# Optimization experiments

Hardware: AMD Instinct MI355X
Metric: run time of the kernel (lower is better)

Reference implementation:

```python
import math
import jax, jax.numpy as jnp
import numpy as np

L = 3
EPS = 1e-06


def _geometry(H, W, L):
    """Replicates the Python-side region layout of the torch ramac() exactly."""
    ovr = 0.4
    steps = np.array([2, 3, 4, 5, 6, 7], dtype=np.float64)
    w = min(W, H)
    b = (max(H, W) - w) / (steps - 1)
    idx = int(np.argmin(np.abs((w ** 2 - w * b) / w ** 2 - ovr)))
    Wd = idx if H < W else 0
    Hd = idx if H > W else 0
    regions = []  # list of (i, j, wl) static ints
    for l in range(1, L + 1):
        wl = math.floor(2 * w / (l + 1))
        if wl == 0:
            continue
        wl2 = math.floor(wl / 2 - 1)
        bW = 0 if l + Wd == 1 else (W - wl) / (l + Wd - 1)
        cenW = [int(math.floor(wl2 + k * bW) - wl2) for k in range(l - 1 + Wd + 1)]
        bH = 0 if l + Hd == 1 else (H - wl) / (l + Hd - 1)
        cenH = [int(math.floor(wl2 + k * bH) - wl2) for k in range(l - 1 + Hd + 1)]
        for i in cenH:
            for j in cenW:
                regions.append((i, j, wl))
    return regions


def _weighted_mac(R, tt_region, eps):
    # R: [B, C, h, w]; tt_region: [B, h, w] bool
    vt = R.max(axis=(2, 3))  # [B, C] regional max-pool
    area = tt_region.shape[-2] * tt_region.shape[-1]
    # NOTE: faithful to torch: sum over batch too, divided only by region area
    wgt = tt_region.sum().astype(jnp.float32) / area
    wgt = jnp.where(wgt <= 1.0 / 3.0, jnp.zeros_like(wgt), wgt)
    nrm = jnp.linalg.norm(vt, axis=1, keepdims=True)  # L2 over channels
    return vt / (nrm + eps) * wgt


def _ramac(x, L, eps):
    B, C, H, W = x.shape
    s = x.sum(axis=1)                 # [B, H, W]
    tt = (s - s.mean()) > 0           # [B, H, W] attention mask (bool)
    v = _weighted_mac(x, tt, eps)     # global region
    for (i, j, wl) in _geometry(H, W, L):
        R = x[:, :, i:i + wl, j:j + wl]
        v = v + _weighted_mac(R, tt[:, i:i + wl, j:j + wl], eps)
    return v.reshape(B, C, 1, 1)


def setup_inputs() -> dict:
    key = jax.random.key(0)
    x = jax.random.normal(key, (16, 1024, 64, 64), dtype=jnp.float32)
    return {"x": x}


def reference(x):
    return _ramac(x, L, EPS)
```

## Files before the change

### kernel.cpp

```cpp
#include <hip/hip_runtime.h>
#include <math.h>


#define NB 16
#define NC 1024
#define HW 4096
#define NF4 1024
#define G 16
#define NCHUNK (NC / G)

template <int ctrl, int rm, int bm>
__device__ __forceinline__ float maxdpp(float x) {
  int xi = __float_as_int(x);
  int yi = __builtin_amdgcn_update_dpp(xi, xi, ctrl, rm, bm, false);
  return fmaxf(x, __int_as_float(yi));
}
__device__ __forceinline__ float wave_max64(float x) {
  x = maxdpp<0x111, 0xf, 0xf>(x);
  x = maxdpp<0x112, 0xf, 0xf>(x);
  x = maxdpp<0x114, 0xf, 0xe>(x);
  x = maxdpp<0x118, 0xf, 0xc>(x);
  x = maxdpp<0x142, 0xa, 0xf>(x);
  x = maxdpp<0x143, 0x8, 0xf>(x);
  return x;
}

__global__ __launch_bounds__(256) void k1_main(
    const float4* __restrict__ x, float* __restrict__ vtp,
    float4* __restrict__ spart4, float* __restrict__ total,
    int* __restrict__ cnt) {
  const int t = threadIdx.x;
  const int chunk = blockIdx.x;
  const int b = blockIdx.y;
  if (chunk == 0 && b == 0) {
    if (t == 0) *total = 0.f;
    if (t < 14) cnt[t] = 0;
  }
  const int fb = t & 15;
  const int r0 = t >> 4;
  const int w = t >> 6;
  const float NEG = -INFINITY;
  const bool cAf = (fb <= 9), cAp = (fb == 10);
  const bool cBf = (fb >= 6), cBp = (fb == 5);
  const bool cCm = (fb < 8);
  const bool cDm = (fb >= 4) && (fb < 12);
  const bool cEm = (fb >= 8);
  const bool rAk2 = (r0 < 10);
  const bool rBk1 = (r0 >= 6);

  float4 sa0 = {0, 0, 0, 0}, sa1 = {0, 0, 0, 0}, sa2 = {0, 0, 0, 0},
         sa3 = {0, 0, 0, 0};
  const float4* img = x + (((size_t)(b * NC + chunk * G)) << 10);

  for (int ci = 0; ci < G; ++ci) {
    const float4* p = img + (((size_t)ci) << 10);
    float4 v0 = p[t], v1 = p[t + 256], v2 = p[t + 512], v3 = p[t + 768];
    sa0.x += v0.x; sa0.y += v0.y; sa0.z += v0.z; sa0.w += v0.w;
    sa1.x += v1.x; sa1.y += v1.y; sa1.z += v1.z; sa1.w += v1.w;
    sa2.x += v2.x; sa2.y += v2.y; sa2.z += v2.z; sa2.w += v2.w;
    sa3.x += v3.x; sa3.y += v3.y; sa3.z += v3.z; sa3.w += v3.w;

    float m0 = fmaxf(fmaxf(v0.x, v0.y), fmaxf(v0.z, v0.w));
    float m1 = fmaxf(fmaxf(v1.x, v1.y), fmaxf(v1.z, v1.w));
    float m2 = fmaxf(fmaxf(v2.x, v2.y), fmaxf(v2.z, v2.w));
    float m3 = fmaxf(fmaxf(v3.x, v3.y), fmaxf(v3.z, v3.w));
    float pA0 = fmaxf(v0.x, v0.y), pA1 = fmaxf(v1.x, v1.y);
    float pA2 = fmaxf(v2.x, v2.y), pA3 = fmaxf(v3.x, v3.y);
    float pB0 = fmaxf(v0.z, v0.w), pB1 = fmaxf(v1.z, v1.w);
    float pB2 = fmaxf(v2.z, v2.w), pB3 = fmaxf(v3.z, v3.w);

    float cA0 = cAf ? m0 : (cAp ? pA0 : NEG);
    float cA1 = cAf ? m1 : (cAp ? pA1 : NEG);
    float cA2 = cAf ? m2 : (cAp ? pA2 : NEG);
    float cA3 = cAf ? m3 : (cAp ? pA3 : NEG);
    float cB0 = cBf ? m0 : (cBp ? pB0 : NEG);
    float cB1 = cBf ? m1 : (cBp ? pB1 : NEG);
    float cB2 = cBf ? m2 : (cBp ? pB2 : NEG);
    float cB3 = cBf ? m3 : (cBp ? pB3 : NEG);
    float cC0 = cCm ? m0 : NEG, cC1 = cCm ? m1 : NEG;
    float cC2 = cCm ? m2 : NEG, cC3 = cCm ? m3 : NEG;
    float cD0 = cDm ? m0 : NEG, cD1 = cDm ? m1 : NEG;
    float cD2 = cDm ? m2 : NEG, cD3 = cDm ? m3 : NEG;
    float cE0 = cEm ? m0 : NEG, cE1 = cEm ? m1 : NEG;
    float cE2 = cEm ? m2 : NEG, cE3 = cEm ? m3 : NEG;

    float g0 = fmaxf(fmaxf(m0, m1), fmaxf(m2, m3));
    float g1 = fmaxf(fmaxf(cA0, cA1), rAk2 ? cA2 : NEG);
    float g2 = fmaxf(fmaxf(cB0, cB1), rAk2 ? cB2 : NEG);
    float g3 = fmaxf(fmaxf(cA2, cA3), rBk1 ? cA1 : NEG);
    float g4 = fmaxf(fmaxf(cB2, cB3), rBk1 ? cB1 : NEG);
    float g5 = fmaxf(cC0, cC1), g6 = fmaxf(cD0, cD1), g7 = fmaxf(cE0, cE1);
    float g8 = fmaxf(cC1, cC2), g9 = fmaxf(cD1, cD2), g10 = fmaxf(cE1, cE2);
    float g11 = fmaxf(cC2, cC3), g12 = fmaxf(cD2, cD3), g13 = fmaxf(cE2, cE3);

    g0 = wave_max64(g0);   g1 = wave_max64(g1);   g2 = wave_max64(g2);
    g3 = wave_max64(g3);   g4 = wave_max64(g4);   g5 = wave_max64(g5);
    g6 = wave_max64(g6);   g7 = wave_max64(g7);   g8 = wave_max64(g8);
    g9 = wave_max64(g9);   g10 = wave_max64(g10); g11 = wave_max64(g11);
    g12 = wave_max64(g12); g13 = wave_max64(g13);

    if ((t & 63) == 63) {
      const int c = chunk * G + ci;
      const int base = ((b << 10) + c) * 4 + w;
      vtp[base]            = g0;  vtp[base + 1 * 65536] = g1;
      vtp[base + 2 * 65536] = g2; vtp[base + 3 * 65536] = g3;
      vtp[base + 4 * 65536] = g4; vtp[base + 5 * 65536] = g5;
      vtp[base + 6 * 65536] = g6; vtp[base + 7 * 65536] = g7;
      vtp[base + 8 * 65536] = g8; vtp[base + 9 * 65536] = g9;
      vtp[base + 10 * 65536] = g10; vtp[base + 11 * 65536] = g11;
      vtp[base + 12 * 65536] = g12; vtp[base + 13 * 65536] = g13;
    }
  }
  const int sb = ((chunk * NB + b) << 10);
  spart4[sb + t] = sa0;
  spart4[sb + t + 256] = sa1;
  spart4[sb + t + 512] = sa2;
  spart4[sb + t + 768] = sa3;
}

__global__ __launch_bounds__(256) void k2_s(const float4* __restrict__ spart4,
                                            float4* __restrict__ s4,
                                            float* __restrict__ total) {
  const int id = blockIdx.x * 256 + threadIdx.x;
  float4 acc = {0, 0, 0, 0};
  for (int ch = 0; ch < NCHUNK; ++ch) {
    float4 v = spart4[(ch << 14) + id];
    acc.x += v.x; acc.y += v.y; acc.z += v.z; acc.w += v.w;
  }
  s4[id] = acc;
  float ts = (acc.x + acc.y) + (acc.z + acc.w);
  for (int off = 1; off < 64; off <<= 1) ts += __shfl_xor(ts, off);
  if ((threadIdx.x & 63) == 0) atomicAdd(total, ts);
}

__global__ __launch_bounds__(256) void k3_cnt(const float* __restrict__ s,
                                              const float* __restrict__ total,
                                              int* __restrict__ cnt) {
  const int b = blockIdx.x;
  const int t = threadIdx.x;
  const float mean = *total * (1.0f / 65536.0f);
  int loc[14];
#pragma unroll
  for (int r = 0; r < 14; ++r) loc[r] = 0;
#pragma unroll
  for (int k = 0; k < 16; ++k) {
    const int p = t + 256 * k;
    const int row = p >> 6, col = p & 63;
    const bool tt = s[(b << 12) + p] > mean;
    if (tt) {
      const bool rA = row < 42, rB = row >= 22, rC = row < 32;
      const bool rD = (row >= 16) && (row < 48), rE = row >= 32;
      const bool cA = col < 42, cB = col >= 22, cC = col < 32;
      const bool cD = (col >= 16) && (col < 48), cE = col >= 32;
      loc[0]++;
      loc[1] += rA && cA;  loc[2] += rA && cB;
      loc[3] += rB && cA;  loc[4] += rB && cB;
      loc[5] += rC && cC;  loc[6] += rC && cD;  loc[7] += rC && cE;
      loc[8] += rD && cC;  loc[9] += rD && cD;  loc[10] += rD && cE;
      loc[11] += rE && cC; loc[12] += rE && cD; loc[13] += rE && cE;
    }
  }
#pragma unroll
  for (int r = 0; r < 14; ++r) {
    int v = loc[r];
    for (int off = 1; off < 64; off <<= 1) v += __shfl_xor(v, off);
    if ((t & 63) == 0) atomicAdd(&cnt[r], v);
  }
}

__global__ __launch_bounds__(256) void k4_vt(const float4* __restrict__ vtp4,
                                             float* __restrict__ vt,
                                             float* __restrict__ nrm) {
  const int rb = blockIdx.x;
  const int t = threadIdx.x;
  float acc = 0.f;
#pragma unroll
  for (int k = 0; k < 4; ++k) {
    const int c = t + 256 * k;
    float4 v = vtp4[(rb << 10) + c];
    float m = fmaxf(fmaxf(v.x, v.y), fmaxf(v.z, v.w));
    vt[(rb << 10) + c] = m;
    acc += m * m;
  }
  for (int off = 1; off < 64; off <<= 1) acc += __shfl_xor(acc, off);
  __shared__ float red[4];
  if ((t & 63) == 0) red[t >> 6] = acc;
  __syncthreads();
  if (t == 0) nrm[rb] = sqrtf(red[0] + red[1] + red[2] + red[3]);
}

__global__ __launch_bounds__(256) void k5_out(const float* __restrict__ vt,
                                              const float* __restrict__ nrm,
                                              const int* __restrict__ cnt,
                                              float* __restrict__ out) {
  const int id = blockIdx.x * 256 + threadIdx.x;
  const int b = id >> 10;
  float acc = 0.f;
#pragma unroll
  for (int r = 0; r < 14; ++r) {
    const float area = (r == 0) ? 4096.f : ((r <= 4) ? 1764.f : 1024.f);
    float wgt = (float)cnt[r] / area;
    if (wgt <= (1.0f / 3.0f)) wgt = 0.f;
    const float mult = (r == 0) ? 2.f : 1.f;
    acc += mult * wgt * vt[r * 16384 + id] / (nrm[r * 16 + b] + 1e-6f);
  }
  out[id] = acc;
}

extern "C" void kernel_launch(void* const* d_in, const int* in_sizes, int n_in,
                              void* d_out, int out_size, void* d_ws,
                              size_t ws_size, hipStream_t stream) {
  const float* x = (const float*)d_in[0];
  float* out = (float*)d_out;

  float* ws = (float*)d_ws;
  float* vtp = ws;
  float* spart = vtp + 917504;
  float* s = spart + 4194304;
  float* vt = s + 65536;
  float* nrm = vt + 229376;
  float* total = nrm + 224;
  int* cnt = (int*)(total + 1);

  k1_main<<<dim3(NCHUNK, NB), 256, 0, stream>>>(
      (const float4*)x, vtp, (float4*)spart, total, cnt);
  k2_s<<<64, 256, 0, stream>>>((const float4*)spart, (float4*)s, total);
  k3_cnt<<<NB, 256, 0, stream>>>(s, total, cnt);
  k4_vt<<<224, 256, 0, stream>>>((const float4*)vtp, vt, nrm);
  k5_out<<<64, 256, 0, stream>>>(vt, nrm, cnt, out);
}
```

Baseline: 392.6 us.

## Stage region maxima in LDS, merge reduction kernels, and simplify region max logic

The main kernel now collects the 14 per-wave regional maxima in shared memory and writes them out as coalesced float4 stores at the end of each block, replacing the scattered scalar global stores. The spatial-sum reduction and the per-region max/norm kernel are merged into one launch that branches on block index, which removes one kernel launch. The per-column masking is also rewritten to combine rows before applying column masks, cutting the number of fmax and select operations. The kernel remains dominated by reading the input, so the gains are limited to launch overhead and store efficiency.

```diff
diff --git a/kernel.cpp b/kernel.cpp
--- a/kernel.cpp
+++ b/kernel.cpp
@@ -4,8 +4,6 @@
 
 #define NB 16
 #define NC 1024
-#define HW 4096
-#define NF4 1024
 #define G 16
 #define NCHUNK (NC / G)
 
@@ -26,7 +24,7 @@
 }
 
 __global__ __launch_bounds__(256) void k1_main(
-    const float4* __restrict__ x, float* __restrict__ vtp,
+    const float4* __restrict__ x, float4* __restrict__ vtp4,
     float4* __restrict__ spart4, float* __restrict__ total,
     int* __restrict__ cnt) {
   const int t = threadIdx.x;
@@ -37,7 +35,7 @@
     if (t < 14) cnt[t] = 0;
   }
   const int fb = t & 15;
-  const int r0 = t >> 4;
+  const int r0t = t >> 4;
   const int w = t >> 6;
   const float NEG = -INFINITY;
   const bool cAf = (fb <= 9), cAp = (fb == 10);
@@ -45,8 +43,10 @@
   const bool cCm = (fb < 8);
   const bool cDm = (fb >= 4) && (fb < 12);
   const bool cEm = (fb >= 8);
-  const bool rAk2 = (r0 < 10);
-  const bool rBk1 = (r0 >= 6);
+  const bool rAk2 = (r0t < 10);
+  const bool rBk1 = (r0t >= 6);
+
+  __shared__ float4 sm4[14][G];
 
   float4 sa0 = {0, 0, 0, 0}, sa1 = {0, 0, 0, 0}, sa2 = {0, 0, 0, 0},
          sa3 = {0, 0, 0, 0};
@@ -69,29 +69,22 @@
     float pB0 = fmaxf(v0.z, v0.w), pB1 = fmaxf(v1.z, v1.w);
     float pB2 = fmaxf(v2.z, v2.w), pB3 = fmaxf(v3.z, v3.w);
 
-    float cA0 = cAf ? m0 : (cAp ? pA0 : NEG);
-    float cA1 = cAf ? m1 : (cAp ? pA1 : NEG);
-    float cA2 = cAf ? m2 : (cAp ? pA2 : NEG);
-    float cA3 = cAf ? m3 : (cAp ? pA3 : NEG);
-    float cB0 = cBf ? m0 : (cBp ? pB0 : NEG);
-    float cB1 = cBf ? m1 : (cBp ? pB1 : NEG);
-    float cB2 = cBf ? m2 : (cBp ? pB2 : NEG);
-    float cB3 = cBf ? m3 : (cBp ? pB3 : NEG);
-    float cC0 = cCm ? m0 : NEG, cC1 = cCm ? m1 : NEG;
-    float cC2 = cCm ? m2 : NEG, cC3 = cCm ? m3 : NEG;
-    float cD0 = cDm ? m0 : NEG, cD1 = cDm ? m1 : NEG;
-    float cD2 = cDm ? m2 : NEG, cD3 = cDm ? m3 : NEG;
-    float cE0 = cEm ? m0 : NEG, cE1 = cEm ? m1 : NEG;
-    float cE2 = cEm ? m2 : NEG, cE3 = cEm ? m3 : NEG;
-
-    float g0 = fmaxf(fmaxf(m0, m1), fmaxf(m2, m3));
-    float g1 = fmaxf(fmaxf(cA0, cA1), rAk2 ? cA2 : NEG);
-    float g2 = fmaxf(fmaxf(cB0, cB1), rAk2 ? cB2 : NEG);
-    float g3 = fmaxf(fmaxf(cA2, cA3), rBk1 ? cA1 : NEG);
-    float g4 = fmaxf(fmaxf(cB2, cB3), rBk1 ? cB1 : NEG);
-    float g5 = fmaxf(cC0, cC1), g6 = fmaxf(cD0, cD1), g7 = fmaxf(cE0, cE1);
-    float g8 = fmaxf(cC1, cC2), g9 = fmaxf(cD1, cD2), g10 = fmaxf(cE1, cE2);
-    float g11 = fmaxf(cC2, cC3), g12 = fmaxf(cD2, cD3), g13 = fmaxf(cE2, cE3);
+    float m01 = fmaxf(m0, m1), m12 = fmaxf(m1, m2), m23 = fmaxf(m2, m3);
+    float MAm = fmaxf(m01, rAk2 ? m2 : NEG);
+    float MBm = fmaxf(m23, rBk1 ? m1 : NEG);
+    float MApA = fmaxf(fmaxf(pA0, pA1), rAk2 ? pA2 : NEG);
+    float MApB = fmaxf(fmaxf(pB0, pB1), rAk2 ? pB2 : NEG);
+    float MBpA = fmaxf(fmaxf(pA2, pA3), rBk1 ? pA1 : NEG);
+    float MBpB = fmaxf(fmaxf(pB2, pB3), rBk1 ? pB1 : NEG);
+
+    float g0 = fmaxf(m01, m23);
+    float g1 = cAf ? MAm : (cAp ? MApA : NEG);
+    float g2 = cBf ? MAm : (cBp ? MApB : NEG);
+    float g3 = cAf ? MBm : (cAp ? MBpA : NEG);
+    float g4 = cBf ? MBm : (cBp ? MBpB : NEG);
+    float g5 = cCm ? m01 : NEG, g6 = cDm ? m01 : NEG, g7 = cEm ? m01 : NEG;
+    float g8 = cCm ? m12 : NEG, g9 = cDm ? m12 : NEG, g10 = cEm ? m12 : NEG;
+    float g11 = cCm ? m23 : NEG, g12 = cDm ? m23 : NEG, g13 = cEm ? m23 : NEG;
 
     g0 = wave_max64(g0);   g1 = wave_max64(g1);   g2 = wave_max64(g2);
     g3 = wave_max64(g3);   g4 = wave_max64(g4);   g5 = wave_max64(g5);
@@ -100,15 +93,15 @@
     g12 = wave_max64(g12); g13 = wave_max64(g13);
 
     if ((t & 63) == 63) {
-      const int c = chunk * G + ci;
-      const int base = ((b << 10) + c) * 4 + w;
-      vtp[base]            = g0;  vtp[base + 1 * 65536] = g1;
-      vtp[base + 2 * 65536] = g2; vtp[base + 3 * 65536] = g3;
-      vtp[base + 4 * 65536] = g4; vtp[base + 5 * 65536] = g5;
-      vtp[base + 6 * 65536] = g6; vtp[base + 7 * 65536] = g7;
-      vtp[base + 8 * 65536] = g8; vtp[base + 9 * 65536] = g9;
-      vtp[base + 10 * 65536] = g10; vtp[base + 11 * 65536] = g11;
-      vtp[base + 12 * 65536] = g12; vtp[base + 13 * 65536] = g13;
+      float* smf = (float*)&sm4[0][0];
+      const int o = (ci << 2) + w;
+      smf[o]               = g0;  smf[o + 1 * (G * 4)] = g1;
+      smf[o + 2 * (G * 4)] = g2;  smf[o + 3 * (G * 4)] = g3;
+      smf[o + 4 * (G * 4)] = g4;  smf[o + 5 * (G * 4)] = g5;
+      smf[o + 6 * (G * 4)] = g6;  smf[o + 7 * (G * 4)] = g7;
+      smf[o + 8 * (G * 4)] = g8;  smf[o + 9 * (G * 4)] = g9;
+      smf[o + 10 * (G * 4)] = g10; smf[o + 11 * (G * 4)] = g11;
+      smf[o + 12 * (G * 4)] = g12; smf[o + 13 * (G * 4)] = g13;
     }
   }
   const int sb = ((chunk * NB + b) << 10);
@@ -116,21 +109,48 @@
   spart4[sb + t + 256] = sa1;
   spart4[sb + t + 512] = sa2;
   spart4[sb + t + 768] = sa3;
-}
-
-__global__ __launch_bounds__(256) void k2_s(const float4* __restrict__ spart4,
-                                            float4* __restrict__ s4,
-                                            float* __restrict__ total) {
-  const int id = blockIdx.x * 256 + threadIdx.x;
-  float4 acc = {0, 0, 0, 0};
-  for (int ch = 0; ch < NCHUNK; ++ch) {
-    float4 v = spart4[(ch << 14) + id];
-    acc.x += v.x; acc.y += v.y; acc.z += v.z; acc.w += v.w;
-  }
-  s4[id] = acc;
-  float ts = (acc.x + acc.y) + (acc.z + acc.w);
-  for (int off = 1; off < 64; off <<= 1) ts += __shfl_xor(ts, off);
-  if ((threadIdx.x & 63) == 0) atomicAdd(total, ts);
+
+  __syncthreads();
+  if (t < 14 * G) {
+    const int r = t >> 4, ci = t & 15;
+    vtp4[r * (NB * NC) + (b << 10) + (chunk << 4) + ci] = sm4[r][ci];
+  }
+}
+
+__global__ __launch_bounds__(256) void k2_mid(
+    const float4* __restrict__ spart4, float4* __restrict__ s4,
+    float* __restrict__ total, const float4* __restrict__ vtp4,
+    float* __restrict__ vt, float* __restrict__ nrm) {
+  const int blk = blockIdx.x;
+  const int t = threadIdx.x;
+  __shared__ float red[4];
+  if (blk < 64) {
+    const int id = blk * 256 + t;
+    float4 acc = {0, 0, 0, 0};
+    for (int ch = 0; ch < NCHUNK; ++ch) {
+      float4 v = spart4[(ch << 14) + id];
+      acc.x += v.x; acc.y += v.y; acc.z += v.z; acc.w += v.w;
+    }
+    s4[id] = acc;
+    float ts = (acc.x + acc.y) + (acc.z + acc.w);
+    for (int off = 1; off < 64; off <<= 1) ts += __shfl_xor(ts, off);
+    if ((t & 63) == 0) atomicAdd(total, ts);
+  } else {
+    const int rb = blk - 64;
+    float acc = 0.f;
+#pragma unroll
+    for (int k = 0; k < 4; ++k) {
+      const int c = t + 256 * k;
+      float4 v = vtp4[(rb << 10) + c];
+      float m = fmaxf(fmaxf(v.x, v.y), fmaxf(v.z, v.w));
+      vt[(rb << 10) + c] = m;
+      acc += m * m;
+    }
+    for (int off = 1; off < 64; off <<= 1) acc += __shfl_xor(acc, off);
+    if ((t & 63) == 0) red[t >> 6] = acc;
+    __syncthreads();
+    if (t == 0) nrm[rb] = sqrtf(red[0] + red[1] + red[2] + red[3]);
+  }
 }
 
 __global__ __launch_bounds__(256) void k3_cnt(const float* __restrict__ s,
@@ -168,28 +188,7 @@
   }
 }
 
-__global__ __launch_bounds__(256) void k4_vt(const float4* __restrict__ vtp4,
-                                             float* __restrict__ vt,
-                                             float* __restrict__ nrm) {
-  const int rb = blockIdx.x;
-  const int t = threadIdx.x;
-  float acc = 0.f;
-#pragma unroll
-  for (int k = 0; k < 4; ++k) {
-    const int c = t + 256 * k;
-    float4 v = vtp4[(rb << 10) + c];
-    float m = fmaxf(fmaxf(v.x, v.y), fmaxf(v.z, v.w));
-    vt[(rb << 10) + c] = m;
-    acc += m * m;
-  }
-  for (int off = 1; off < 64; off <<= 1) acc += __shfl_xor(acc, off);
-  __shared__ float red[4];
-  if ((t & 63) == 0) red[t >> 6] = acc;
-  __syncthreads();
-  if (t == 0) nrm[rb] = sqrtf(red[0] + red[1] + red[2] + red[3]);
-}
-
-__global__ __launch_bounds__(256) void k5_out(const float* __restrict__ vt,
+__global__ __launch_bounds__(256) void k4_out(const float* __restrict__ vt,
                                               const float* __restrict__ nrm,
                                               const int* __restrict__ cnt,
                                               float* __restrict__ out) {
@@ -223,9 +222,9 @@
   int* cnt = (int*)(total + 1);
 
   k1_main<<<dim3(NCHUNK, NB), 256, 0, stream>>>(
-      (const float4*)x, vtp, (float4*)spart, total, cnt);
-  k2_s<<<64, 256, 0, stream>>>((const float4*)spart, (float4*)s, total);
+      (const float4*)x, (float4*)vtp, (float4*)spart, total, cnt);
+  k2_mid<<<64 + 224, 256, 0, stream>>>((const float4*)spart, (float4*)s, total,
+                                       (const float4*)vtp, vt, nrm);
   k3_cnt<<<NB, 256, 0, stream>>>(s, total, cnt);
-  k4_vt<<<224, 256, 0, stream>>>((const float4*)vtp, vt, nrm);
-  k5_out<<<64, 256, 0, stream>>>(vt, nrm, cnt, out);
-}
+  k4_out<<<64, 256, 0, stream>>>(vt, nrm, cnt, out);
+}
```

Result: no change. 390.0 us (-0.7%).
